# Optimization experiments

Hardware: AMD Instinct MI355X
Metric: run time of the kernel (lower is better)

Reference implementation:

```python
import jax, jax.numpy as jnp
import numpy as np

B, Q, K, H, D = 2, 2048, 2048, 16, 64


def setup_inputs() -> dict:
    key = jax.random.key(0)
    k1, k2, k3, k4 = jax.random.split(key, 4)
    qs = jax.random.normal(k1, (B, Q, H, D), dtype=jnp.float32)
    ks = jax.random.normal(k2, (B, K, H, D), dtype=jnp.float32)
    vs = jax.random.normal(k3, (B, K, H, D), dtype=jnp.float32)
    # valid lengths in [1, K] so no row is fully masked
    valid_lens = jax.random.randint(k4, (B,), 1, K + 1, dtype=jnp.int32)
    return {"qs": qs, "ks": ks, "vs": vs, "valid_lens": valid_lens}


def reference(qs, ks, vs, valid_lens):
    # Flash-attention-2 scan computes exact softmax attention with key masking;
    # the dense, numerically-stable equivalent:
    d = qs.shape[-1]
    scale = 1.0 / jnp.sqrt(jnp.asarray(d, dtype=qs.dtype))
    # scores: [B, H, Q, K]
    scores = jnp.einsum("bqhd,bkhd->bhqk", qs * scale, ks)
    kpos = jnp.arange(ks.shape[1])
    ks_mask = kpos[None, :] < valid_lens[:, None]            # [B, K]
    scores = jnp.where(ks_mask[:, None, None, :], scores, -jnp.inf)
    attn = jax.nn.softmax(scores, axis=-1)                   # stable online-softmax equivalent
    out = jnp.einsum("bhqk,bkhd->bqhd", attn, vs)            # [B, Q, H, D]
    return out
```

## Files before the change

kernel.cpp:

```cpp
#include <hip/hip_runtime.h>

#define B_ 2
#define Q_ 2048
#define K_ 2048
#define H_ 16
#define D_ 64
#define HD_ (H_ * D_)

#define QSCALE 0.18033688011112042f
#define DEFER_THR 10.0f

typedef __bf16 bf16_t;
typedef __attribute__((ext_vector_type(8))) __bf16 bf16x8;
typedef __attribute__((ext_vector_type(4))) __bf16 bf16x4;
typedef __attribute__((ext_vector_type(4))) float f32x4;
typedef __attribute__((ext_vector_type(4))) unsigned int u32x4;

#define SBAR() do {                                         \
    __builtin_amdgcn_sched_barrier(0);                      \
    asm volatile("s_waitcnt lgkmcnt(0)" ::: "memory");      \
    __builtin_amdgcn_s_barrier();                           \
    __builtin_amdgcn_sched_barrier(0);                      \
} while (0)

__device__ __forceinline__ int swz(int row, int colByte) {
    return (row * 128 + colByte) ^ ((row & 7) << 4);
}

__global__ __launch_bounds__(512) void attn_fwd_kernel(
    const float* __restrict__ qs, const float* __restrict__ ks,
    const float* __restrict__ vs, const int* __restrict__ valid_lens,
    float* __restrict__ out)
{
    const int qt   = blockIdx.x;
    const int h    = blockIdx.y;
    const int b    = blockIdx.z;
    const int tid  = threadIdx.x;
    const int lane = tid & 63;
    const int l16  = lane & 15;
    const int lhi  = lane >> 4;

    const int valid  = valid_lens[b];
    const int ntiles = (valid + 63) >> 6;

    __shared__ bf16_t k_lds[2][64 * 64];
    __shared__ bf16_t v_lds[2][64 * 64];

    const int    qrow = qt * 128 + (tid >> 6) * 16 + l16;
    const float* qp   = qs + (((size_t)b * Q_ + qrow) * H_ + h) * D_;
    bf16x8 a_q[2];
    #pragma unroll
    for (int dh = 0; dh < 2; ++dh) {
        const f32x4* q4 = (const f32x4*)(qp + dh * 32 + lhi * 8);
        f32x4 lo = q4[0], hi = q4[1];
        #pragma unroll
        for (int j = 0; j < 4; ++j) {
            a_q[dh][j]     = (bf16_t)(lo[j] * QSCALE);
            a_q[dh][4 + j] = (bf16_t)(hi[j] * QSCALE);
        }
    }

    f32x4 o_acc[4];
    #pragma unroll
    for (int t = 0; t < 4; ++t) o_acc[t] = (f32x4){0.f, 0.f, 0.f, 0.f};
    float m_r = -1e30f, l_part = 0.f;

    const float* kb = ks + ((size_t)b * K_ * H_ + h) * D_;
    const float* vg = vs + ((size_t)b * K_ * H_ + h) * D_;

    const bool kRole = (tid < 256);
    const int  st    = kRole ? tid : (tid - 256);
    const int  krow  = st >> 2;
    const int  kcolf = (st & 3) * 16;
    const int  vr    = (st & 15) * 4;
    const int  vc    = (st >> 4) * 4;

    f32x4 reg[4];

    auto issue_loads = [&](int kt) {
        if (kRole) {
            const float* ksrc = kb + (size_t)(kt * 64 + krow) * HD_ + kcolf;
            #pragma unroll
            for (int i = 0; i < 4; ++i) reg[i] = ((const f32x4*)ksrc)[i];
        } else {
            #pragma unroll
            for (int i = 0; i < 4; ++i)
                reg[i] = *(const f32x4*)(vg + (size_t)(kt * 64 + vr + i) * HD_ + vc);
        }
    };

    auto write_tile = [&](int bi) {
        if (kRole) {
            char* kdst = (char*)&k_lds[bi][0];
            bf16x8 lo, hi;
            #pragma unroll
            for (int j = 0; j < 4; ++j) {
                lo[j] = (bf16_t)reg[0][j]; lo[4 + j] = (bf16_t)reg[1][j];
                hi[j] = (bf16_t)reg[2][j]; hi[4 + j] = (bf16_t)reg[3][j];
            }
            *(bf16x8*)(kdst + swz(krow, kcolf * 2))      = lo;
            *(bf16x8*)(kdst + swz(krow, kcolf * 2 + 16)) = hi;
        } else {
            char* vdst = (char*)&v_lds[bi][0];
            #pragma unroll
            for (int j = 0; j < 4; ++j) {
                bf16x4 w;
                w[0] = (bf16_t)reg[0][j]; w[1] = (bf16_t)reg[1][j];
                w[2] = (bf16_t)reg[2][j]; w[3] = (bf16_t)reg[3][j];
                *(bf16x4*)(vdst + swz(vc + j, vr * 2)) = w;
            }
        }
    };

    issue_loads(0);
    write_tile(0);
    int cur = 0;

    for (int kt = 0; kt < ntiles; ++kt) {
        const bool more = (kt + 1 < ntiles);
        if (more) issue_loads(kt + 1);
        SBAR();

        char* const kbase = (char*)&k_lds[cur][0];
        char* const vbase = (char*)&v_lds[cur][0];

        f32x4 s[4];
        #pragma unroll
        for (int n = 0; n < 4; ++n) s[n] = (f32x4){0.f, 0.f, 0.f, 0.f};
        __builtin_amdgcn_s_setprio(1);
        #pragma unroll
        for (int n = 0; n < 4; ++n) {
            #pragma unroll
            for (int dh = 0; dh < 2; ++dh) {
                bf16x8 ak = *(const bf16x8*)(kbase + swz(n * 16 + l16, dh * 64 + lhi * 16));
                s[n] = __builtin_amdgcn_mfma_f32_16x16x32_bf16(ak, a_q[dh], s[n], 0, 0, 0);
            }
        }
        __builtin_amdgcn_s_setprio(0);

        if (kt * 64 + 64 > valid) {
            #pragma unroll
            for (int n = 0; n < 4; ++n) {
                const int kbase_i = kt * 64 + n * 16 + lhi * 4;
                #pragma unroll
                for (int r = 0; r < 4; ++r)
                    if (kbase_i + r >= valid) s[n][r] = -1e30f;
            }
        }

        float lm = s[0][0];
        #pragma unroll
        for (int n = 0; n < 4; ++n)
            #pragma unroll
            for (int r = 0; r < 4; ++r) lm = fmaxf(lm, s[n][r]);
        if (__any(lm > m_r + DEFER_THR)) {
            float rm = fmaxf(lm, __shfl_xor(lm, 16, 64));
            rm = fmaxf(rm, __shfl_xor(rm, 32, 64));
            const float mnew  = fmaxf(m_r, rm);
            const float alpha = __builtin_amdgcn_exp2f(m_r - mnew);
            m_r = mnew;
            l_part *= alpha;
            #pragma unroll
            for (int t = 0; t < 4; ++t) o_acc[t] *= alpha;
        }

        bf16x8 pb[2];
        {
            float psum = 0.f;
            unsigned pk[4][2];
            #pragma unroll
            for (int n = 0; n < 4; ++n) {
                float e0 = __builtin_amdgcn_exp2f(s[n][0] - m_r);
                float e1 = __builtin_amdgcn_exp2f(s[n][1] - m_r);
                float e2 = __builtin_amdgcn_exp2f(s[n][2] - m_r);
                float e3 = __builtin_amdgcn_exp2f(s[n][3] - m_r);
                psum += (e0 + e1) + (e2 + e3);
                asm("v_cvt_pk_bf16_f32 %0, %1, %2" : "=v"(pk[n][0]) : "v"(e0), "v"(e1));
                asm("v_cvt_pk_bf16_f32 %0, %1, %2" : "=v"(pk[n][1]) : "v"(e2), "v"(e3));
            }
            l_part += psum;
            #pragma unroll
            for (int kk = 0; kk < 2; ++kk) {
                unsigned a0 = pk[2 * kk][0],     a1 = pk[2 * kk][1];
                unsigned b0 = pk[2 * kk + 1][0], b1 = pk[2 * kk + 1][1];
                asm("v_permlane32_swap_b32 %0, %1" : "+v"(a0), "+v"(b0));
                asm("v_permlane16_swap_b32 %0, %1" : "+v"(a0), "+v"(b0));
                asm("v_permlane32_swap_b32 %0, %1" : "+v"(a1), "+v"(b1));
                asm("v_permlane16_swap_b32 %0, %1" : "+v"(a1), "+v"(b1));
                u32x4 words = {a0, a1, b0, b1};
                pb[kk] = __builtin_bit_cast(bf16x8, words);
            }
        }

        __builtin_amdgcn_s_setprio(1);
        #pragma unroll
        for (int t = 0; t < 4; ++t) {
            #pragma unroll
            for (int kk = 0; kk < 2; ++kk) {
                bf16x8 vb = *(const bf16x8*)(vbase + swz(t * 16 + l16, kk * 64 + lhi * 16));
                o_acc[t] = __builtin_amdgcn_mfma_f32_16x16x32_bf16(vb, pb[kk], o_acc[t], 0, 0, 0);
            }
        }
        __builtin_amdgcn_s_setprio(0);

        if (more) write_tile(cur ^ 1);
        cur ^= 1;
    }

    float l = l_part;
    l += __shfl_xor(l, 16, 64);
    l += __shfl_xor(l, 32, 64);
    const float inv = 1.f / l;
    float* op = out + (((size_t)b * Q_ + qrow) * H_ + h) * D_;
    #pragma unroll
    for (int t = 0; t < 4; ++t) {
        f32x4 res = o_acc[t];
        #pragma unroll
        for (int r = 0; r < 4; ++r) res[r] *= inv;
        *(f32x4*)(op + t * 16 + lhi * 4) = res;
    }
}

extern "C" void kernel_launch(void* const* d_in, const int* in_sizes, int n_in,
                              void* d_out, int out_size, void* d_ws, size_t ws_size,
                              hipStream_t stream) {
    const float* qs = (const float*)d_in[0];
    const float* ks = (const float*)d_in[1];
    const float* vs = (const float*)d_in[2];
    const int*   vl = (const int*)d_in[3];
    float*       out = (float*)d_out;
    attn_fwd_kernel<<<dim3(Q_ / 128, H_, B_), 512, 0, stream>>>(qs, ks, vs, vl, out);
}
```

Baseline: 36.99 us.

## Split softmax and PV into two 32-key halves for interleaving

Each 64-key tile's softmax and PV product now run as two 32-key halves, each with its own max check, exp, pack and four MFMAs. The aim is to let the exp/VALU work of one half overlap the PV MFMAs of the other and to shorten dependency chains. The cost is a second deferred-rescale check per tile, which can add extra rescales of the accumulators. The exponent reference also changes more often, which can slightly alter numerics.

```diff
diff --git a/kernel.cpp b/kernel.cpp
--- a/kernel.cpp
+++ b/kernel.cpp
@@ -148,60 +148,103 @@
             }
         }
 
-        float lm = s[0][0];
-        #pragma unroll
-        for (int n = 0; n < 4; ++n)
-            #pragma unroll
-            for (int r = 0; r < 4; ++r) lm = fmaxf(lm, s[n][r]);
-        if (__any(lm > m_r + DEFER_THR)) {
-            float rm = fmaxf(lm, __shfl_xor(lm, 16, 64));
-            rm = fmaxf(rm, __shfl_xor(rm, 32, 64));
-            const float mnew  = fmaxf(m_r, rm);
-            const float alpha = __builtin_amdgcn_exp2f(m_r - mnew);
-            m_r = mnew;
-            l_part *= alpha;
-            #pragma unroll
-            for (int t = 0; t < 4; ++t) o_acc[t] *= alpha;
-        }
-
-        bf16x8 pb[2];
         {
+            float lm = fmaxf(fmaxf(s[0][0], s[0][1]), fmaxf(s[0][2], s[0][3]));
+            lm = fmaxf(fmaxf(lm, s[1][0]), fmaxf(s[1][1], fmaxf(s[1][2], s[1][3])));
+            if (__any(lm > m_r + DEFER_THR)) {
+                float rm = fmaxf(lm, __shfl_xor(lm, 16, 64));
+                rm = fmaxf(rm, __shfl_xor(rm, 32, 64));
+                const float mnew  = fmaxf(m_r, rm);
+                const float alpha = __builtin_amdgcn_exp2f(m_r - mnew);
+                m_r = mnew;
+                l_part *= alpha;
+                #pragma unroll
+                for (int t = 0; t < 4; ++t) o_acc[t] *= alpha;
+            }
             float psum = 0.f;
-            unsigned pk[4][2];
-            #pragma unroll
-            for (int n = 0; n < 4; ++n) {
-                float e0 = __builtin_amdgcn_exp2f(s[n][0] - m_r);
-                float e1 = __builtin_amdgcn_exp2f(s[n][1] - m_r);
-                float e2 = __builtin_amdgcn_exp2f(s[n][2] - m_r);
-                float e3 = __builtin_amdgcn_exp2f(s[n][3] - m_r);
+            unsigned pk0[2], pk1[2];
+            {
+                float e0 = __builtin_amdgcn_exp2f(s[0][0] - m_r);
+                float e1 = __builtin_amdgcn_exp2f(s[0][1] - m_r);
+                float e2 = __builtin_amdgcn_exp2f(s[0][2] - m_r);
+                float e3 = __builtin_amdgcn_exp2f(s[0][3] - m_r);
                 psum += (e0 + e1) + (e2 + e3);
-                asm("v_cvt_pk_bf16_f32 %0, %1, %2" : "=v"(pk[n][0]) : "v"(e0), "v"(e1));
-                asm("v_cvt_pk_bf16_f32 %0, %1, %2" : "=v"(pk[n][1]) : "v"(e2), "v"(e3));
+                asm("v_cvt_pk_bf16_f32 %0, %1, %2" : "=v"(pk0[0]) : "v"(e0), "v"(e1));
+                asm("v_cvt_pk_bf16_f32 %0, %1, %2" : "=v"(pk0[1]) : "v"(e2), "v"(e3));
+                float f0 = __builtin_amdgcn_exp2f(s[1][0] - m_r);
+                float f1 = __builtin_amdgcn_exp2f(s[1][1] - m_r);
+                float f2 = __builtin_amdgcn_exp2f(s[1][2] - m_r);
+                float f3 = __builtin_amdgcn_exp2f(s[1][3] - m_r);
+                psum += (f0 + f1) + (f2 + f3);
+                asm("v_cvt_pk_bf16_f32 %0, %1, %2" : "=v"(pk1[0]) : "v"(f0), "v"(f1));
+                asm("v_cvt_pk_bf16_f32 %0, %1, %2" : "=v"(pk1[1]) : "v"(f2), "v"(f3));
             }
             l_part += psum;
-            #pragma unroll
-            for (int kk = 0; kk < 2; ++kk) {
-                unsigned a0 = pk[2 * kk][0],     a1 = pk[2 * kk][1];
-                unsigned b0 = pk[2 * kk + 1][0], b1 = pk[2 * kk + 1][1];
-                asm("v_permlane32_swap_b32 %0, %1" : "+v"(a0), "+v"(b0));
-                asm("v_permlane16_swap_b32 %0, %1" : "+v"(a0), "+v"(b0));
-                asm("v_permlane32_swap_b32 %0, %1" : "+v"(a1), "+v"(b1));
-                asm("v_permlane16_swap_b32 %0, %1" : "+v"(a1), "+v"(b1));
-                u32x4 words = {a0, a1, b0, b1};
-                pb[kk] = __builtin_bit_cast(bf16x8, words);
-            }
-        }
-
-        __builtin_amdgcn_s_setprio(1);
-        #pragma unroll
-        for (int t = 0; t < 4; ++t) {
-            #pragma unroll
-            for (int kk = 0; kk < 2; ++kk) {
-                bf16x8 vb = *(const bf16x8*)(vbase + swz(t * 16 + l16, kk * 64 + lhi * 16));
-                o_acc[t] = __builtin_amdgcn_mfma_f32_16x16x32_bf16(vb, pb[kk], o_acc[t], 0, 0, 0);
-            }
-        }
-        __builtin_amdgcn_s_setprio(0);
+            unsigned a0 = pk0[0], a1 = pk0[1], b0 = pk1[0], b1 = pk1[1];
+            asm("v_permlane32_swap_b32 %0, %1" : "+v"(a0), "+v"(b0));
+            asm("v_permlane16_swap_b32 %0, %1" : "+v"(a0), "+v"(b0));
+            asm("v_permlane32_swap_b32 %0, %1" : "+v"(a1), "+v"(b1));
+            asm("v_permlane16_swap_b32 %0, %1" : "+v"(a1), "+v"(b1));
+            u32x4 words = {a0, a1, b0, b1};
+            bf16x8 pb = __builtin_bit_cast(bf16x8, words);
+
+            __builtin_amdgcn_s_setprio(1);
+            #pragma unroll
+            for (int t = 0; t < 4; ++t) {
+                bf16x8 vb = *(const bf16x8*)(vbase + swz(t * 16 + l16, lhi * 16));
+                o_acc[t] = __builtin_amdgcn_mfma_f32_16x16x32_bf16(vb, pb, o_acc[t], 0, 0, 0);
+            }
+            __builtin_amdgcn_s_setprio(0);
+        }
+
+        {
+            float lm = fmaxf(fmaxf(s[2][0], s[2][1]), fmaxf(s[2][2], s[2][3]));
+            lm = fmaxf(fmaxf(lm, s[3][0]), fmaxf(s[3][1], fmaxf(s[3][2], s[3][3])));
+            if (__any(lm > m_r + DEFER_THR)) {
+                float rm = fmaxf(lm, __shfl_xor(lm, 16, 64));
+                rm = fmaxf(rm, __shfl_xor(rm, 32, 64));
+                const float mnew  = fmaxf(m_r, rm);
+                const float alpha = __builtin_amdgcn_exp2f(m_r - mnew);
+                m_r = mnew;
+                l_part *= alpha;
+                #pragma unroll
+                for (int t = 0; t < 4; ++t) o_acc[t] *= alpha;
+            }
+            float psum = 0.f;
+            unsigned pk0[2], pk1[2];
+            {
+                float e0 = __builtin_amdgcn_exp2f(s[2][0] - m_r);
+                float e1 = __builtin_amdgcn_exp2f(s[2][1] - m_r);
+                float e2 = __builtin_amdgcn_exp2f(s[2][2] - m_r);
+                float e3 = __builtin_amdgcn_exp2f(s[2][3] - m_r);
+                psum += (e0 + e1) + (e2 + e3);
+                asm("v_cvt_pk_bf16_f32 %0, %1, %2" : "=v"(pk0[0]) : "v"(e0), "v"(e1));
+                asm("v_cvt_pk_bf16_f32 %0, %1, %2" : "=v"(pk0[1]) : "v"(e2), "v"(e3));
+                float f0 = __builtin_amdgcn_exp2f(s[3][0] - m_r);
+                float f1 = __builtin_amdgcn_exp2f(s[3][1] - m_r);
+                float f2 = __builtin_amdgcn_exp2f(s[3][2] - m_r);
+                float f3 = __builtin_amdgcn_exp2f(s[3][3] - m_r);
+                psum += (f0 + f1) + (f2 + f3);
+                asm("v_cvt_pk_bf16_f32 %0, %1, %2" : "=v"(pk1[0]) : "v"(f0), "v"(f1));
+                asm("v_cvt_pk_bf16_f32 %0, %1, %2" : "=v"(pk1[1]) : "v"(f2), "v"(f3));
+            }
+            l_part += psum;
+            unsigned a0 = pk0[0], a1 = pk0[1], b0 = pk1[0], b1 = pk1[1];
+            asm("v_permlane32_swap_b32 %0, %1" : "+v"(a0), "+v"(b0));
+            asm("v_permlane16_swap_b32 %0, %1" : "+v"(a0), "+v"(b0));
+            asm("v_permlane32_swap_b32 %0, %1" : "+v"(a1), "+v"(b1));
+            asm("v_permlane16_swap_b32 %0, %1" : "+v"(a1), "+v"(b1));
+            u32x4 words = {a0, a1, b0, b1};
+            bf16x8 pb = __builtin_bit_cast(bf16x8, words);
+
+            __builtin_amdgcn_s_setprio(1);
+            #pragma unroll
+            for (int t = 0; t < 4; ++t) {
+                bf16x8 vb = *(const bf16x8*)(vbase + swz(t * 16 + l16, 64 + lhi * 16));
+                o_acc[t] = __builtin_amdgcn_mfma_f32_16x16x32_bf16(vb, pb, o_acc[t], 0, 0, 0);
+            }
+            __builtin_amdgcn_s_setprio(0);
+        }
 
         if (more) write_tile(cur ^ 1);
         cur ^= 1;
```

Result: slower. 38.70 us (+4.6%).
